# Kernel tuning notes

Hardware: AMD Instinct MI355X
Metric: run time of the kernel (lower is better)

Reference implementation:

```python
import math
import jax, jax.numpy as jnp
import numpy as np

ROPE_DIMS = 16  # rope applied to last 16 channels only
N_WIN = 16      # sliding window size


def rmsnorm(x, w):
    return x * jax.lax.rsqrt(jnp.mean(x * x, axis=-1, keepdims=True) + 1e-8) * w


def apply_rope(x, negate=False):
    # x: [B, H, T, C]; rotate last ROPE_DIMS channels with interleaved pairs
    T = x.shape[2]
    x_pass, x_rope = x[..., :-ROPE_DIMS], x[..., -ROPE_DIMS:]
    t = jnp.arange(T, dtype=x.dtype)
    if negate:
        t = -t
    k = jnp.arange(ROPE_DIMS // 2, dtype=x.dtype)
    theta = 10000.0 ** (-2.0 * k / ROPE_DIMS)          # [8]
    freqs = t[:, None] * theta[None, :]                 # [T, 8]
    cos, sin = jnp.cos(freqs), jnp.sin(freqs)
    x1, x2 = x_rope[..., 0::2], x_rope[..., 1::2]
    rx1 = x1 * cos - x2 * sin
    rx2 = x1 * sin + x2 * cos
    rx = jnp.stack([rx1, rx2], axis=-1).reshape(x_rope.shape)
    return jnp.concatenate([x_pass, rx], axis=-1)


def setup_inputs() -> dict:
    key = jax.random.key(0)
    ks = jax.random.split(key, 14)
    B, T, d, c, nh = 4, 2048, 256, 64, 4
    s = 0.02
    return {
        "H": jax.random.normal(ks[0], (B, T, d), jnp.float32),
        "W_Q": jax.random.normal(ks[1], (nh * c, d), jnp.float32) * s,
        "W_K": jax.random.normal(ks[2], (c, d), jnp.float32) * s,
        "W_V": jax.random.normal(ks[3], (c, d), jnp.float32) * s,
        "wq": 1.0 + 0.1 * jax.random.normal(ks[4], (nh, c), jnp.float32),
        "wk": 1.0 + 0.1 * jax.random.normal(ks[5], (c,), jnp.float32),
        "wv": 1.0 + 0.1 * jax.random.normal(ks[6], (c,), jnp.float32),
        "Wg0": jax.random.normal(ks[7], (64, 2 * c), jnp.float32) * s,
        "bg0": jnp.zeros((64,), jnp.float32),
        "Wg1": jax.random.normal(ks[8], (64, 2 * c), jnp.float32) * s,
        "bg1": jnp.zeros((64,), jnp.float32),
        "Wout": jax.random.normal(ks[9], (d, 128), jnp.float32) * s,
        "bout": jnp.zeros((d,), jnp.float32),
    }


def reference(H, W_Q, W_K, W_V, wq, wk, wv, Wg0, bg0, Wg1, bg1, Wout, bout):
    B, T, d = H.shape
    nh, c = wq.shape
    # projections
    Q = (H @ W_Q.T).reshape(B, T, nh, c).transpose(0, 2, 1, 3)   # [B,nh,T,c]
    K = (H @ W_K.T)[:, None]                                      # [B,1,T,c]
    V = (H @ W_V.T)[:, None]                                      # [B,1,T,c]
    # per-head RMSNorm on Q, shared RMSNorm on K/V
    Q = rmsnorm(Q, wq[None, :, None, :])
    K = rmsnorm(K, wk)
    V = rmsnorm(V, wv)
    # partial RoPE (last 16 dims); V is also rotated in this module
    Q = apply_rope(Q)
    K = apply_rope(K)[:, 0]                                       # [B,T,c]
    V = apply_rope(V)[:, 0]
    # dense scores with sliding-window causal mask (width N_WIN)
    S = jnp.einsum('bhtc,bsc->bhts', Q, K) / math.sqrt(c)
    i = jnp.arange(T)[:, None]
    j = jnp.arange(T)[None, :]
    allowed = (j <= i) & (j >= i - (N_WIN - 1))                   # [T,T]
    S = jnp.where(allowed, S, -jnp.inf)
    P = jax.nn.softmax(S, axis=-1)
    O = jnp.einsum('bhts,bsc->bhtc', P, V)                        # [B,nh,T,c]
    O = apply_rope(O, negate=True)
    # group heads {0,1} and {2,3}
    O_g0 = O[:, :2].transpose(0, 2, 1, 3).reshape(B, T, 2 * c)
    O_g1 = O[:, 2:].transpose(0, 2, 1, 3).reshape(B, T, 2 * c)
    p0 = O_g0 @ Wg0.T + bg0
    p1 = O_g1 @ Wg1.T + bg1
    p_all = jnp.concatenate([p0, p1], axis=-1)                    # [B,T,128]
    return p_all @ Wout.T + bout
```

## Files before the change

kernel.cpp:

```cpp
#include <hip/hip_runtime.h>
#include <math.h>

#define T_SEQ 2048
#define DMODEL 256
#define C_HEAD 64
#define NH 4
#define NWIN 16
#define B_SZ 4

typedef __attribute__((ext_vector_type(8))) short bf16x8;
typedef __attribute__((ext_vector_type(8))) unsigned short ushort8;
typedef __attribute__((ext_vector_type(4))) float f32x4;

static __device__ __forceinline__ unsigned short f2bf(float f) {
    union { float f; unsigned int u; } v; v.f = f;
    unsigned int r = v.u + 0x7FFFu + ((v.u >> 16) & 1u);
    return (unsigned short)(r >> 16);
}

__global__ __launch_bounds__(256) void conv_w_kernel(
    const float* __restrict__ WQ, const float* __restrict__ WK,
    const float* __restrict__ WV, const float* __restrict__ Wg0,
    const float* __restrict__ Wg1, const float* __restrict__ Wout,
    unsigned short* __restrict__ dst, float2* __restrict__ rtab) {
    const int tid = threadIdx.x;
    if (blockIdx.x >= 72) {
        const int idx = (blockIdx.x - 72) * 256 + tid;
        const int t = idx >> 3, k = idx & 7;
        const float theta = powf(10000.0f, -0.125f * (float)k);
        const float fr = (float)t * theta;
        rtab[idx] = make_float2(cosf(fr), sinf(fr));
        return;
    }
    const int i = blockIdx.x * 256 + tid;
    const float* s; long off; long doff;
    if (i < 12288) {
        const long e = (long)i * 8;
        const int col = (int)(e >> 8), k = (int)(e & 255);
        if      (col < 256) { s = WQ; off = (long)col * 256 + k; }
        else if (col < 320) { s = WK; off = (long)(col - 256) * 256 + k; }
        else                { s = WV; off = (long)(col - 320) * 256 + k; }
        doff = ((long)(col >> 4) * 8 + (k >> 5)) * 512 + ((k >> 3) & 3) * 128 + (col & 15) * 8;
    } else {
        const long e = (long)(i - 12288) * 8;
        const int col = (int)(e >> 7), k = (int)(e & 127);
        if      (col < 64)  { s = Wg0; off = (long)col * 128 + k; }
        else if (col < 128) { s = Wg1; off = (long)(col - 64) * 128 + k; }
        else                { s = Wout; off = (long)(col - 128) * 128 + k; }
        doff = 98304 + ((long)(col >> 4) * 4 + (k >> 5)) * 512 + ((k >> 3) & 3) * 128 + (col & 15) * 8;
    }
    const float4* s4 = (const float4*)(s + off);
    float4 a = s4[0], b = s4[1];
    ushort8 o;
    o[0] = f2bf(a.x); o[1] = f2bf(a.y); o[2] = f2bf(a.z); o[3] = f2bf(a.w);
    o[4] = f2bf(b.x); o[5] = f2bf(b.y); o[6] = f2bf(b.z); o[7] = f2bf(b.w);
    *(ushort8*)(dst + doff) = o;
}

__global__ __launch_bounds__(1024) void fused_kernel(
    const float* __restrict__ H, const unsigned short* __restrict__ Wallb,
    const float* __restrict__ wq, const float* __restrict__ wk,
    const float* __restrict__ wv, const float2* __restrict__ rtab,
    const float* __restrict__ bg0, const float* __restrict__ bg1,
    const float* __restrict__ bout, float* __restrict__ out)
{
    __shared__ __align__(16) char smem[62464];
    char* lds_a = smem;
    char* o_lds = smem;
    char* p_lds = smem + 16384;
    char* q_lds = smem + 24576;
    char* k_lds = smem + 40960;
    char* v_t   = smem + 47104;
    char* p_att = smem + 54272;

    const int tid = threadIdx.x;
    const int blk = blockIdx.x;
    const int b  = blk >> 6;
    const int t0 = (blk & 63) << 5;

    const unsigned short* Wpk2 = Wallb + 98304;

    for (int idx = tid; idx < 1536; idx += 1024) {
        int row = idx >> 5, ch = idx & 31;
        int t = t0 - 16 + row; if (t < 0) t = 0;
        const float4* s4 = (const float4*)(H + ((size_t)b * T_SEQ + t) * DMODEL + ch * 8);
        float4 a = s4[0], c = s4[1];
        ushort8 o;
        o[0] = f2bf(a.x); o[1] = f2bf(a.y); o[2] = f2bf(a.z); o[3] = f2bf(a.w);
        o[4] = f2bf(c.x); o[5] = f2bf(c.y); o[6] = f2bf(c.z); o[7] = f2bf(c.w);
        int byte = row * 512 + ch * 16;
        byte ^= (row & 7) << 4;
        *(ushort8*)(lds_a + byte) = o;
    }
    __syncthreads();

    const int w  = tid >> 6;
    const int l  = tid & 63;
    const int g  = l >> 4;
    const int li = l & 15;
    const int lane16 = l * 8;

    if (w < 8) {
        const int h  = w >> 1;
        const int th = w & 1;
        f32x4 acc[4] = {};
        #pragma unroll
        for (int ks = 0; ks < 8; ++ks) {
            const int row = 16 + th * 16 + li;
            int byte = row * 512 + (ks * 32 + g * 8) * 2;
            byte ^= (row & 7) << 4;
            bf16x8 a = *(const bf16x8*)(lds_a + byte);
            #pragma unroll
            for (int nf = 0; nf < 4; ++nf) {
                bf16x8 bq = *(const bf16x8*)(Wallb + (size_t)((h * 4 + nf) * 8 + ks) * 512 + lane16);
                acc[nf] = __builtin_amdgcn_mfma_f32_16x16x32_bf16(a, bq, acc[nf], 0, 0, 0);
            }
        }
        float gw[4];
        #pragma unroll
        for (int nf = 0; nf < 4; ++nf) gw[nf] = wq[h * 64 + nf * 16 + li];
        #pragma unroll
        for (int r = 0; r < 4; ++r) {
            float x0 = acc[0][r], x1 = acc[1][r];
            float x2 = acc[2][r], x3 = acc[3][r];
            float ss = x0 * x0 + x1 * x1 + x2 * x2 + x3 * x3;
            ss += __shfl_xor(ss, 1);
            ss += __shfl_xor(ss, 2);
            ss += __shfl_xor(ss, 4);
            ss += __shfl_xor(ss, 8);
            const float rinv = rsqrtf(ss * (1.0f / 64.0f) + 1e-8f);
            const int tok = th * 16 + g * 4 + r;
            const int t = t0 + tok;
            float v0 = x0 * rinv * gw[0];
            float v1 = x1 * rinv * gw[1];
            float v2 = x2 * rinv * gw[2];
            float v3 = x3 * rinv * gw[3];
            float2 cs = rtab[t * 8 + (li >> 1)];
            float px = __shfl_xor(v3, 1);
            v3 = ((li & 1) == 0) ? (v3 * cs.x - px * cs.y) : (px * cs.y + v3 * cs.x);
            char* qb = q_lds + h * 4096;
            const int sw = (tok & 7) << 4;
            *(unsigned short*)(qb + ((tok * 128 + (0 * 16 + li) * 2) ^ sw)) = f2bf(v0);
            *(unsigned short*)(qb + ((tok * 128 + (1 * 16 + li) * 2) ^ sw)) = f2bf(v1);
            *(unsigned short*)(qb + ((tok * 128 + (2 * 16 + li) * 2) ^ sw)) = f2bf(v2);
            *(unsigned short*)(qb + ((tok * 128 + (3 * 16 + li) * 2) ^ sw)) = f2bf(v3);
        }
    } else if (w < 14) {
        const int idx  = w - 8;
        const int sel  = (idx >= 3) ? 1 : 0;
        const int slab = sel ? (idx - 3) : idx;
        f32x4 acc[4] = {};
        #pragma unroll
        for (int ks = 0; ks < 8; ++ks) {
            const int row = slab * 16 + li;
            int byte = row * 512 + (ks * 32 + g * 8) * 2;
            byte ^= (row & 7) << 4;
            bf16x8 a = *(const bf16x8*)(lds_a + byte);
            #pragma unroll
            for (int nf = 0; nf < 4; ++nf) {
                bf16x8 bkv = *(const bf16x8*)(Wallb + (size_t)((16 + sel * 4 + nf) * 8 + ks) * 512 + lane16);
                acc[nf] = __builtin_amdgcn_mfma_f32_16x16x32_bf16(a, bkv, acc[nf], 0, 0, 0);
            }
        }
        float gw[4];
        #pragma unroll
        for (int nf = 0; nf < 4; ++nf)
            gw[nf] = (sel == 0) ? wk[nf * 16 + li] : wv[nf * 16 + li];
        #pragma unroll
        for (int r = 0; r < 4; ++r) {
            float x0 = acc[0][r], x1 = acc[1][r];
            float x2 = acc[2][r], x3 = acc[3][r];
            float ss = x0 * x0 + x1 * x1 + x2 * x2 + x3 * x3;
            ss += __shfl_xor(ss, 1);
            ss += __shfl_xor(ss, 2);
            ss += __shfl_xor(ss, 4);
            ss += __shfl_xor(ss, 8);
            const float rinv = rsqrtf(ss * (1.0f / 64.0f) + 1e-8f);
            const int row = slab * 16 + g * 4 + r;
            int tk = t0 - 16 + row; if (tk < 0) tk = 0;
            float v0 = x0 * rinv * gw[0];
            float v1 = x1 * rinv * gw[1];
            float v2 = x2 * rinv * gw[2];
            float v3 = x3 * rinv * gw[3];
            float2 cs = rtab[tk * 8 + (li >> 1)];
            float px = __shfl_xor(v3, 1);
            v3 = ((li & 1) == 0) ? (v3 * cs.x - px * cs.y) : (px * cs.y + v3 * cs.x);
            if (sel == 0) {
                const int sw = (row & 7) << 4;
                *(unsigned short*)(k_lds + ((row * 128 + (0 * 16 + li) * 2) ^ sw)) = f2bf(v0);
                *(unsigned short*)(k_lds + ((row * 128 + (1 * 16 + li) * 2) ^ sw)) = f2bf(v1);
                *(unsigned short*)(k_lds + ((row * 128 + (2 * 16 + li) * 2) ^ sw)) = f2bf(v2);
                *(unsigned short*)(k_lds + ((row * 128 + (3 * 16 + li) * 2) ^ sw)) = f2bf(v3);
            } else {
                *(unsigned short*)(v_t + (0 * 16 + li) * 112 + row * 2) = f2bf(v0);
                *(unsigned short*)(v_t + (1 * 16 + li) * 112 + row * 2) = f2bf(v1);
                *(unsigned short*)(v_t + (2 * 16 + li) * 112 + row * 2) = f2bf(v2);
                *(unsigned short*)(v_t + (3 * 16 + li) * 112 + row * 2) = f2bf(v3);
            }
        }
    }
    __syncthreads();

    if (w < 8) {
        const int h  = w >> 1;
        const int th = w & 1;
        bf16x8 qf0, qf1;
        {
            const char* qb = q_lds + h * 4096;
            const int tok = th * 16 + li;
            const int sw = (tok & 7) << 4;
            qf0 = *(const bf16x8*)(qb + ((tok * 128 + g * 16) ^ sw));
            qf1 = *(const bf16x8*)(qb + ((tok * 128 + 64 + g * 16) ^ sw));
        }
        f32x4 st[2];
        #pragma unroll
        for (int tile = 0; tile < 2; ++tile) {
            const int row = th * 16 + tile * 16 + li;
            const int sw = (row & 7) << 4;
            bf16x8 kf0 = *(const bf16x8*)(k_lds + ((row * 128 + g * 16) ^ sw));
            bf16x8 kf1 = *(const bf16x8*)(k_lds + ((row * 128 + 64 + g * 16) ^ sw));
            f32x4 acc = {};
            acc = __builtin_amdgcn_mfma_f32_16x16x32_bf16(kf0, qf0, acc, 0, 0, 0);
            acc = __builtin_amdgcn_mfma_f32_16x16x32_bf16(kf1, qf1, acc, 0, 0, 0);
            st[tile] = acc;
        }

        float p[8];
        float mx = -1e30f;
        #pragma unroll
        for (int tile = 0; tile < 2; ++tile) {
            #pragma unroll
            for (int r = 0; r < 4; ++r) {
                int krel = tile * 16 - 16 + g * 4 + r;
                int dd = li - krel;
                bool ok = ((unsigned)dd < 16u) && (t0 + th * 16 + krel >= 0);
                float v = ok ? st[tile][r] * 0.125f : -1e30f;
                p[tile * 4 + r] = v;
                mx = fmaxf(mx, v);
            }
        }
        mx = fmaxf(mx, __shfl_xor(mx, 16));
        mx = fmaxf(mx, __shfl_xor(mx, 32));
        float sum = 0.f;
        #pragma unroll
        for (int i = 0; i < 8; ++i) { p[i] = __expf(p[i] - mx); sum += p[i]; }
        sum += __shfl_xor(sum, 16);
        sum += __shfl_xor(sum, 32);
        const float inv = 1.0f / sum;

        bf16x8 paf;
        {
            char* pbase = p_att + w * 1024;
            uint2 w0, w1;
            w0.x = (unsigned)f2bf(p[0] * inv) | ((unsigned)f2bf(p[1] * inv) << 16);
            w0.y = (unsigned)f2bf(p[2] * inv) | ((unsigned)f2bf(p[3] * inv) << 16);
            w1.x = (unsigned)f2bf(p[4] * inv) | ((unsigned)f2bf(p[5] * inv) << 16);
            w1.y = (unsigned)f2bf(p[6] * inv) | ((unsigned)f2bf(p[7] * inv) << 16);
            const int sw = (li & 3) << 4;
            *(uint2*)(pbase + ((li * 64 + 0 * 32 + g * 8) ^ sw)) = w0;
            *(uint2*)(pbase + ((li * 64 + 1 * 32 + g * 8) ^ sw)) = w1;
            asm volatile("s_waitcnt lgkmcnt(0)" ::: "memory");
            paf = *(const bf16x8*)(pbase + ((li * 64 + g * 16) ^ sw));
        }

        f32x4 o[4] = {};
        #pragma unroll
        for (int ctile = 0; ctile < 4; ++ctile) {
            bf16x8 vf = *(const bf16x8*)(v_t + (ctile * 16 + li) * 112 + th * 32 + g * 16);
            o[ctile] = __builtin_amdgcn_mfma_f32_16x16x32_bf16(paf, vf, o[ctile], 0, 0, 0);
        }

        #pragma unroll
        for (int r = 0; r < 4; ++r) {
            const int row = th * 16 + g * 4 + r;
            const int t = t0 + row;
            float o3 = o[3][r];
            float po = __shfl_xor(o3, 1);
            float2 cs = rtab[t * 8 + (li >> 1)];
            o3 = ((li & 1) == 0) ? (o3 * cs.x + po * cs.y) : (-po * cs.y + o3 * cs.x);
            #pragma unroll
            for (int ctile = 0; ctile < 4; ++ctile) {
                const int col = h * 64 + ctile * 16 + li;
                int byte = row * 512 + col * 2;
                byte ^= (row & 7) << 4;
                float val = (ctile == 3) ? o3 : o[ctile][r];
                *(unsigned short*)(o_lds + byte) = f2bf(val);
            }
        }
    }
    __syncthreads();

    {
        const int gate = (w >> 3) & 1, colq = (w >> 1) & 3, rh = w & 1;
        const float* bg = gate ? bg1 : bg0;
        f32x4 accp = {};
        #pragma unroll
        for (int ks = 0; ks < 4; ++ks) {
            const int row = rh * 16 + li;
            int byte = row * 512 + (gate * 128 + ks * 32 + g * 8) * 2;
            byte ^= (row & 7) << 4;
            bf16x8 a = *(const bf16x8*)(o_lds + byte);
            const int colblk = gate * 4 + colq;
            bf16x8 bfr = *(const bf16x8*)(Wpk2 + (size_t)(colblk * 4 + ks) * 512 + lane16);
            accp = __builtin_amdgcn_mfma_f32_16x16x32_bf16(a, bfr, accp, 0, 0, 0);
        }
        const int cl = colq * 16 + li;
        const int pcol = gate * 64 + cl;
        const float bb = bg[cl];
        #pragma unroll
        for (int r = 0; r < 4; ++r) {
            const int row = rh * 16 + g * 4 + r;
            int byte = row * 256 + pcol * 2;
            byte ^= (row & 7) << 4;
            *(unsigned short*)(p_lds + byte) = f2bf(accp[r] + bb);
        }
    }
    __syncthreads();

    {
        f32x4 acco[2] = {};
        #pragma unroll
        for (int ks = 0; ks < 4; ++ks) {
            bf16x8 a[2];
            #pragma unroll
            for (int mf = 0; mf < 2; ++mf) {
                const int row = mf * 16 + li;
                int byte = row * 256 + (ks * 32 + g * 8) * 2;
                byte ^= (row & 7) << 4;
                a[mf] = *(const bf16x8*)(p_lds + byte);
            }
            const int colblk = 8 + w;
            bf16x8 bfr = *(const bf16x8*)(Wpk2 + (size_t)(colblk * 4 + ks) * 512 + lane16);
            acco[0] = __builtin_amdgcn_mfma_f32_16x16x32_bf16(a[0], bfr, acco[0], 0, 0, 0);
            acco[1] = __builtin_amdgcn_mfma_f32_16x16x32_bf16(a[1], bfr, acco[1], 0, 0, 0);
        }
        const int col = w * 16 + li;
        const float bb = bout[col];
        #pragma unroll
        for (int mf = 0; mf < 2; ++mf) {
            #pragma unroll
            for (int r = 0; r < 4; ++r) {
                const int row = mf * 16 + g * 4 + r;
                out[(size_t)(b * T_SEQ + t0 + row) * DMODEL + col] = acco[mf][r] + bb;
            }
        }
    }
}

extern "C" void kernel_launch(void* const* d_in, const int* in_sizes, int n_in,
                              void* d_out, int out_size, void* d_ws, size_t ws_size,
                              hipStream_t stream) {
    const float* H    = (const float*)d_in[0];
    const float* WQ   = (const float*)d_in[1];
    const float* WK   = (const float*)d_in[2];
    const float* WV   = (const float*)d_in[3];
    const float* wq   = (const float*)d_in[4];
    const float* wk   = (const float*)d_in[5];
    const float* wv   = (const float*)d_in[6];
    const float* Wg0  = (const float*)d_in[7];
    const float* bg0  = (const float*)d_in[8];
    const float* Wg1  = (const float*)d_in[9];
    const float* bg1  = (const float*)d_in[10];
    const float* Wout = (const float*)d_in[11];
    const float* bout = (const float*)d_in[12];
    float* out = (float*)d_out;

    char* ws = (char*)d_ws;
    unsigned short* Wallb = (unsigned short*)ws;
    float2* rtab = (float2*)(ws + 294912);

    conv_w_kernel<<<136, 256, 0, stream>>>(WQ, WK, WV, Wg0, Wg1, Wout, Wallb, rtab);
    fused_kernel<<<B_SZ * T_SEQ / 32, 1024, 0, stream>>>(H, Wallb, wq, wk, wv, rtab,
                                                         bg0, bg1, bout, out);
}
```

Baseline: 22.11 us.

## Prefetch weight fragments into registers ahead of barriers and MFMA loops

Global weight fragments for the QKV projection are now loaded two k-steps ahead in a register pipeline, and the first fragments are issued before the first barrier so they overlap the H-to-LDS staging. Gate and output projection weights are prefetched into registers during earlier phases so that the later GEMMs wait only on LDS. __syncthreads is replaced with a custom barrier that waits only on LDS counters, which lets global prefetches stay in flight across barriers. The rope table's powf is also replaced with constants. This raises register pressure and depends on correct vmem/lgkm counter handling.

```diff
diff --git a/kernel.cpp b/kernel.cpp
--- a/kernel.cpp
+++ b/kernel.cpp
@@ -11,6 +11,8 @@
 typedef __attribute__((ext_vector_type(8))) short bf16x8;
 typedef __attribute__((ext_vector_type(8))) unsigned short ushort8;
 typedef __attribute__((ext_vector_type(4))) float f32x4;
+
+#define BAR() asm volatile("s_waitcnt lgkmcnt(0)\n\ts_barrier" ::: "memory")
 
 static __device__ __forceinline__ unsigned short f2bf(float f) {
     union { float f; unsigned int u; } v; v.f = f;
@@ -25,10 +27,13 @@
     unsigned short* __restrict__ dst, float2* __restrict__ rtab) {
     const int tid = threadIdx.x;
     if (blockIdx.x >= 72) {
+        const float th_tab[8] = {1.f, 0.31622776601683794f, 0.1f,
+                                 0.03162277660168379f, 0.01f,
+                                 0.0031622776601683794f, 0.001f,
+                                 0.00031622776601683794f};
         const int idx = (blockIdx.x - 72) * 256 + tid;
         const int t = idx >> 3, k = idx & 7;
-        const float theta = powf(10000.0f, -0.125f * (float)k);
-        const float fr = (float)t * theta;
+        const float fr = (float)t * th_tab[k];
         rtab[idx] = make_float2(cosf(fr), sinf(fr));
         return;
     }
@@ -80,6 +85,24 @@
 
     const unsigned short* Wpk2 = Wallb + 98304;
 
+    const int w  = tid >> 6;
+    const int l  = tid & 63;
+    const int g  = l >> 4;
+    const int li = l & 15;
+    const int lane16 = l * 8;
+
+    const int sel  = (w >= 11) ? 1 : 0;
+    const int slab = (w >= 11) ? (w - 11) : (w - 8);
+    int cb0, rowa;
+    if (w < 8)       { cb0 = (w >> 1) * 4; rowa = 16 + (w & 1) * 16 + li; }
+    else if (w < 14) { cb0 = 16 + sel * 4; rowa = slab * 16 + li; }
+    else             { cb0 = 0;            rowa = li; }
+
+#define WFRAG(nf, ks) (*(const bf16x8*)(Wallb + (size_t)((cb0 + (nf)) * 8 + (ks)) * 512 + lane16))
+
+    const int gate = (w >> 3) & 1, colq = (w >> 1) & 3, rh = w & 1;
+    bf16x8 gpre[4];
+
     for (int idx = tid; idx < 1536; idx += 1024) {
         int row = idx >> 5, ch = idx & 31;
         int t = t0 - 16 + row; if (t < 0) t = 0;
@@ -92,115 +115,113 @@
         byte ^= (row & 7) << 4;
         *(ushort8*)(lds_a + byte) = o;
     }
-    __syncthreads();
-
-    const int w  = tid >> 6;
-    const int l  = tid & 63;
-    const int g  = l >> 4;
-    const int li = l & 15;
-    const int lane16 = l * 8;
-
-    if (w < 8) {
-        const int h  = w >> 1;
-        const int th = w & 1;
+    bf16x8 cur[4], nxt[4];
+    if (w < 14) {
+        #pragma unroll
+        for (int nf = 0; nf < 4; ++nf) { cur[nf] = WFRAG(nf, 0); nxt[nf] = WFRAG(nf, 1); }
+    } else {
+        #pragma unroll
+        for (int ks = 0; ks < 4; ++ks)
+            gpre[ks] = *(const bf16x8*)(Wpk2 + (size_t)((gate * 4 + colq) * 4 + ks) * 512 + lane16);
+    }
+    BAR();
+
+    if (w < 14) {
         f32x4 acc[4] = {};
         #pragma unroll
         for (int ks = 0; ks < 8; ++ks) {
-            const int row = 16 + th * 16 + li;
-            int byte = row * 512 + (ks * 32 + g * 8) * 2;
-            byte ^= (row & 7) << 4;
-            bf16x8 a = *(const bf16x8*)(lds_a + byte);
-            #pragma unroll
-            for (int nf = 0; nf < 4; ++nf) {
-                bf16x8 bq = *(const bf16x8*)(Wallb + (size_t)((h * 4 + nf) * 8 + ks) * 512 + lane16);
-                acc[nf] = __builtin_amdgcn_mfma_f32_16x16x32_bf16(a, bq, acc[nf], 0, 0, 0);
-            }
-        }
-        float gw[4];
-        #pragma unroll
-        for (int nf = 0; nf < 4; ++nf) gw[nf] = wq[h * 64 + nf * 16 + li];
-        #pragma unroll
-        for (int r = 0; r < 4; ++r) {
-            float x0 = acc[0][r], x1 = acc[1][r];
-            float x2 = acc[2][r], x3 = acc[3][r];
-            float ss = x0 * x0 + x1 * x1 + x2 * x2 + x3 * x3;
-            ss += __shfl_xor(ss, 1);
-            ss += __shfl_xor(ss, 2);
-            ss += __shfl_xor(ss, 4);
-            ss += __shfl_xor(ss, 8);
-            const float rinv = rsqrtf(ss * (1.0f / 64.0f) + 1e-8f);
-            const int tok = th * 16 + g * 4 + r;
-            const int t = t0 + tok;
-            float v0 = x0 * rinv * gw[0];
-            float v1 = x1 * rinv * gw[1];
-            float v2 = x2 * rinv * gw[2];
-            float v3 = x3 * rinv * gw[3];
-            float2 cs = rtab[t * 8 + (li >> 1)];
-            float px = __shfl_xor(v3, 1);
-            v3 = ((li & 1) == 0) ? (v3 * cs.x - px * cs.y) : (px * cs.y + v3 * cs.x);
-            char* qb = q_lds + h * 4096;
-            const int sw = (tok & 7) << 4;
-            *(unsigned short*)(qb + ((tok * 128 + (0 * 16 + li) * 2) ^ sw)) = f2bf(v0);
-            *(unsigned short*)(qb + ((tok * 128 + (1 * 16 + li) * 2) ^ sw)) = f2bf(v1);
-            *(unsigned short*)(qb + ((tok * 128 + (2 * 16 + li) * 2) ^ sw)) = f2bf(v2);
-            *(unsigned short*)(qb + ((tok * 128 + (3 * 16 + li) * 2) ^ sw)) = f2bf(v3);
-        }
-    } else if (w < 14) {
-        const int idx  = w - 8;
-        const int sel  = (idx >= 3) ? 1 : 0;
-        const int slab = sel ? (idx - 3) : idx;
-        f32x4 acc[4] = {};
-        #pragma unroll
-        for (int ks = 0; ks < 8; ++ks) {
-            const int row = slab * 16 + li;
-            int byte = row * 512 + (ks * 32 + g * 8) * 2;
-            byte ^= (row & 7) << 4;
-            bf16x8 a = *(const bf16x8*)(lds_a + byte);
-            #pragma unroll
-            for (int nf = 0; nf < 4; ++nf) {
-                bf16x8 bkv = *(const bf16x8*)(Wallb + (size_t)((16 + sel * 4 + nf) * 8 + ks) * 512 + lane16);
-                acc[nf] = __builtin_amdgcn_mfma_f32_16x16x32_bf16(a, bkv, acc[nf], 0, 0, 0);
-            }
-        }
-        float gw[4];
-        #pragma unroll
-        for (int nf = 0; nf < 4; ++nf)
-            gw[nf] = (sel == 0) ? wk[nf * 16 + li] : wv[nf * 16 + li];
-        #pragma unroll
-        for (int r = 0; r < 4; ++r) {
-            float x0 = acc[0][r], x1 = acc[1][r];
-            float x2 = acc[2][r], x3 = acc[3][r];
-            float ss = x0 * x0 + x1 * x1 + x2 * x2 + x3 * x3;
-            ss += __shfl_xor(ss, 1);
-            ss += __shfl_xor(ss, 2);
-            ss += __shfl_xor(ss, 4);
-            ss += __shfl_xor(ss, 8);
-            const float rinv = rsqrtf(ss * (1.0f / 64.0f) + 1e-8f);
-            const int row = slab * 16 + g * 4 + r;
-            int tk = t0 - 16 + row; if (tk < 0) tk = 0;
-            float v0 = x0 * rinv * gw[0];
-            float v1 = x1 * rinv * gw[1];
-            float v2 = x2 * rinv * gw[2];
-            float v3 = x3 * rinv * gw[3];
-            float2 cs = rtab[tk * 8 + (li >> 1)];
-            float px = __shfl_xor(v3, 1);
-            v3 = ((li & 1) == 0) ? (v3 * cs.x - px * cs.y) : (px * cs.y + v3 * cs.x);
-            if (sel == 0) {
-                const int sw = (row & 7) << 4;
-                *(unsigned short*)(k_lds + ((row * 128 + (0 * 16 + li) * 2) ^ sw)) = f2bf(v0);
-                *(unsigned short*)(k_lds + ((row * 128 + (1 * 16 + li) * 2) ^ sw)) = f2bf(v1);
-                *(unsigned short*)(k_lds + ((row * 128 + (2 * 16 + li) * 2) ^ sw)) = f2bf(v2);
-                *(unsigned short*)(k_lds + ((row * 128 + (3 * 16 + li) * 2) ^ sw)) = f2bf(v3);
-            } else {
-                *(unsigned short*)(v_t + (0 * 16 + li) * 112 + row * 2) = f2bf(v0);
-                *(unsigned short*)(v_t + (1 * 16 + li) * 112 + row * 2) = f2bf(v1);
-                *(unsigned short*)(v_t + (2 * 16 + li) * 112 + row * 2) = f2bf(v2);
-                *(unsigned short*)(v_t + (3 * 16 + li) * 112 + row * 2) = f2bf(v3);
-            }
-        }
-    }
-    __syncthreads();
-
+            bf16x8 fut[4];
+            if (ks < 6) {
+                #pragma unroll
+                for (int nf = 0; nf < 4; ++nf) fut[nf] = WFRAG(nf, ks + 2);
+            }
+            int abyte = rowa * 512 + (ks * 32 + g * 8) * 2;
+            abyte ^= (rowa & 7) << 4;
+            bf16x8 a = *(const bf16x8*)(lds_a + abyte);
+            #pragma unroll
+            for (int nf = 0; nf < 4; ++nf)
+                acc[nf] = __builtin_amdgcn_mfma_f32_16x16x32_bf16(a, cur[nf], acc[nf], 0, 0, 0);
+            #pragma unroll
+            for (int nf = 0; nf < 4; ++nf) { cur[nf] = nxt[nf]; nxt[nf] = fut[nf]; }
+        }
+
+        if (w < 8) {
+            const int h = w >> 1;
+            float gw[4];
+            #pragma unroll
+            for (int nf = 0; nf < 4; ++nf) gw[nf] = wq[h * 64 + nf * 16 + li];
+            #pragma unroll
+            for (int r = 0; r < 4; ++r) {
+                float x0 = acc[0][r], x1 = acc[1][r];
+                float x2 = acc[2][r], x3 = acc[3][r];
+                float ss = x0 * x0 + x1 * x1 + x2 * x2 + x3 * x3;
+                ss += __shfl_xor(ss, 1);
+                ss += __shfl_xor(ss, 2);
+                ss += __shfl_xor(ss, 4);
+                ss += __shfl_xor(ss, 8);
+                const float rinv = rsqrtf(ss * (1.0f / 64.0f) + 1e-8f);
+                const int tok = (w & 1) * 16 + g * 4 + r;
+                const int t = t0 + tok;
+                float v0 = x0 * rinv * gw[0];
+                float v1 = x1 * rinv * gw[1];
+                float v2 = x2 * rinv * gw[2];
+                float v3 = x3 * rinv * gw[3];
+                float2 cs = rtab[t * 8 + (li >> 1)];
+                float px = __shfl_xor(v3, 1);
+                v3 = ((li & 1) == 0) ? (v3 * cs.x - px * cs.y) : (px * cs.y + v3 * cs.x);
+                char* qb = q_lds + h * 4096;
+                const int sw = (tok & 7) << 4;
+                *(unsigned short*)(qb + ((tok * 128 + (0 * 16 + li) * 2) ^ sw)) = f2bf(v0);
+                *(unsigned short*)(qb + ((tok * 128 + (1 * 16 + li) * 2) ^ sw)) = f2bf(v1);
+                *(unsigned short*)(qb + ((tok * 128 + (2 * 16 + li) * 2) ^ sw)) = f2bf(v2);
+                *(unsigned short*)(qb + ((tok * 128 + (3 * 16 + li) * 2) ^ sw)) = f2bf(v3);
+            }
+        } else {
+            float gw[4];
+            #pragma unroll
+            for (int nf = 0; nf < 4; ++nf)
+                gw[nf] = (sel == 0) ? wk[nf * 16 + li] : wv[nf * 16 + li];
+            #pragma unroll
+            for (int r = 0; r < 4; ++r) {
+                float x0 = acc[0][r], x1 = acc[1][r];
+                float x2 = acc[2][r], x3 = acc[3][r];
+                float ss = x0 * x0 + x1 * x1 + x2 * x2 + x3 * x3;
+                ss += __shfl_xor(ss, 1);
+                ss += __shfl_xor(ss, 2);
+                ss += __shfl_xor(ss, 4);
+                ss += __shfl_xor(ss, 8);
+                const float rinv = rsqrtf(ss * (1.0f / 64.0f) + 1e-8f);
+                const int row = slab * 16 + g * 4 + r;
+                int tk = t0 - 16 + row; if (tk < 0) tk = 0;
+                float v0 = x0 * rinv * gw[0];
+                float v1 = x1 * rinv * gw[1];
+                float v2 = x2 * rinv * gw[2];
+                float v3 = x3 * rinv * gw[3];
+                float2 cs = rtab[tk * 8 + (li >> 1)];
+                float px = __shfl_xor(v3, 1);
+                v3 = ((li & 1) == 0) ? (v3 * cs.x - px * cs.y) : (px * cs.y + v3 * cs.x);
+                if (sel == 0) {
+                    const int sw = (row & 7) << 4;
+                    *(unsigned short*)(k_lds + ((row * 128 + (0 * 16 + li) * 2) ^ sw)) = f2bf(v0);
+                    *(unsigned short*)(k_lds + ((row * 128 + (1 * 16 + li) * 2) ^ sw)) = f2bf(v1);
+                    *(unsigned short*)(k_lds + ((row * 128 + (2 * 16 + li) * 2) ^ sw)) = f2bf(v2);
+                    *(unsigned short*)(k_lds + ((row * 128 + (3 * 16 + li) * 2) ^ sw)) = f2bf(v3);
+                } else {
+                    *(unsigned short*)(v_t + (0 * 16 + li) * 112 + row * 2) = f2bf(v0);
+                    *(unsigned short*)(v_t + (1 * 16 + li) * 112 + row * 2) = f2bf(v1);
+                    *(unsigned short*)(v_t + (2 * 16 + li) * 112 + row * 2) = f2bf(v2);
+                    *(unsigned short*)(v_t + (3 * 16 + li) * 112 + row * 2) = f2bf(v3);
+                }
+            }
+        }
+    }
+    BAR();
+
+    if (w >= 8 && w < 14) {
+        #pragma unroll
+        for (int ks = 0; ks < 4; ++ks)
+            gpre[ks] = *(const bf16x8*)(Wpk2 + (size_t)((gate * 4 + colq) * 4 + ks) * 512 + lane16);
+    }
     if (w < 8) {
         const int h  = w >> 1;
         const int th = w & 1;
@@ -219,10 +240,10 @@
             const int sw = (row & 7) << 4;
             bf16x8 kf0 = *(const bf16x8*)(k_lds + ((row * 128 + g * 16) ^ sw));
             bf16x8 kf1 = *(const bf16x8*)(k_lds + ((row * 128 + 64 + g * 16) ^ sw));
-            f32x4 acc = {};
-            acc = __builtin_amdgcn_mfma_f32_16x16x32_bf16(kf0, qf0, acc, 0, 0, 0);
-            acc = __builtin_amdgcn_mfma_f32_16x16x32_bf16(kf1, qf1, acc, 0, 0, 0);
-            st[tile] = acc;
+            f32x4 sa = {};
+            sa = __builtin_amdgcn_mfma_f32_16x16x32_bf16(kf0, qf0, sa, 0, 0, 0);
+            sa = __builtin_amdgcn_mfma_f32_16x16x32_bf16(kf1, qf1, sa, 0, 0, 0);
+            st[tile] = sa;
         }
 
         float p[8];
@@ -287,11 +308,14 @@
                 *(unsigned short*)(o_lds + byte) = f2bf(val);
             }
         }
-    }
-    __syncthreads();
-
+        #pragma unroll
+        for (int ks = 0; ks < 4; ++ks)
+            gpre[ks] = *(const bf16x8*)(Wpk2 + (size_t)((gate * 4 + colq) * 4 + ks) * 512 + lane16);
+    }
+    BAR();
+
+    bf16x8 opre[4];
     {
-        const int gate = (w >> 3) & 1, colq = (w >> 1) & 3, rh = w & 1;
         const float* bg = gate ? bg1 : bg0;
         f32x4 accp = {};
         #pragma unroll
@@ -300,10 +324,11 @@
             int byte = row * 512 + (gate * 128 + ks * 32 + g * 8) * 2;
             byte ^= (row & 7) << 4;
             bf16x8 a = *(const bf16x8*)(o_lds + byte);
-            const int colblk = gate * 4 + colq;
-            bf16x8 bfr = *(const bf16x8*)(Wpk2 + (size_t)(colblk * 4 + ks) * 512 + lane16);
-            accp = __builtin_amdgcn_mfma_f32_16x16x32_bf16(a, bfr, accp, 0, 0, 0);
-        }
+            accp = __builtin_amdgcn_mfma_f32_16x16x32_bf16(a, gpre[ks], accp, 0, 0, 0);
+        }
+        #pragma unroll
+        for (int ks = 0; ks < 4; ++ks)
+            opre[ks] = *(const bf16x8*)(Wpk2 + (size_t)((8 + w) * 4 + ks) * 512 + lane16);
         const int cl = colq * 16 + li;
         const int pcol = gate * 64 + cl;
         const float bb = bg[cl];
@@ -315,7 +340,7 @@
             *(unsigned short*)(p_lds + byte) = f2bf(accp[r] + bb);
         }
     }
-    __syncthreads();
+    BAR();
 
     {
         f32x4 acco[2] = {};
@@ -329,10 +354,8 @@
                 byte ^= (row & 7) << 4;
                 a[mf] = *(const bf16x8*)(p_lds + byte);
             }
-            const int colblk = 8 + w;
-            bf16x8 bfr = *(const bf16x8*)(Wpk2 + (size_t)(colblk * 4 + ks) * 512 + lane16);
-            acco[0] = __builtin_amdgcn_mfma_f32_16x16x32_bf16(a[0], bfr, acco[0], 0, 0, 0);
-            acco[1] = __builtin_amdgcn_mfma_f32_16x16x32_bf16(a[1], bfr, acco[1], 0, 0, 0);
+            acco[0] = __builtin_amdgcn_mfma_f32_16x16x32_bf16(a[0], opre[ks], acco[0], 0, 0, 0);
+            acco[1] = __builtin_amdgcn_mfma_f32_16x16x32_bf16(a[1], opre[ks], acco[1], 0, 0, 0);
         }
         const int col = w * 16 + li;
         const float bb = bout[col];
@@ -345,6 +368,7 @@
             }
         }
     }
+#undef WFRAG
 }
 
 extern "C" void kernel_launch(void* const* d_in, const int* in_sizes, int n_in,
```

New measurement: 21.02 us, median of 2. 1.05x faster.
